# Optimization experiments

Hardware: AMD Instinct MI355X
Metric: run time of the kernel (lower is better)

## Reference

```python
import jax, jax.numpy as jnp
import numpy as np

N = 50000    # total nodes in a batched graph
E = 200000   # directed edges (before self loops)
G = 256      # molecules per batch
F_IN = 64    # atom features
H = 4        # gat heads
CH = 128     # hidden_channels (per head)
D = H * CH   # 512, concat width
MLP_H = 128  # hidden_channels * mlp_hidden_factor
NEG_SLOPE = 0.2


def _gat(x, src, dst, W, a_src, a_dst, b, concat):
    """PyG GATConv (eval mode, self loops already added to src/dst)."""
    n = x.shape[0]
    heads, ch = a_src.shape
    h = (x @ W).reshape(n, heads, ch)                       # [N,H,C]
    e = jax.nn.leaky_relu((h * a_src).sum(-1)[src]
                          + (h * a_dst).sum(-1)[dst], NEG_SLOPE)  # [E,H]
    emax = jax.ops.segment_max(e, dst, num_segments=n)
    emax = jnp.where(jnp.isfinite(emax), emax, 0.0)
    p = jnp.exp(e - emax[dst])
    denom = jax.ops.segment_sum(p, dst, num_segments=n)
    alpha = p / (denom[dst] + 1e-16)                        # segment softmax over dst
    out = jax.ops.segment_sum(h[src] * alpha[..., None], dst, num_segments=n)
    out = out.reshape(n, heads * ch) if concat else out.mean(axis=1)
    return out + b


def _encoder(x, edge_index, batch, p):
    n = x.shape[0]
    loop = jnp.arange(n, dtype=edge_index.dtype)            # GATConv add_self_loops=True
    src = jnp.concatenate([edge_index[0], loop])
    dst = jnp.concatenate([edge_index[1], loop])
    x = jax.nn.elu(_gat(x, src, dst, p['W1'], p['as1'], p['ad1'], p['b1'], True))
    x = jax.nn.elu(_gat(x, src, dst, p['W2'], p['as2'], p['ad2'], p['b2'], True))
    x = _gat(x, src, dst, p['W3'], p['as3'], p['ad3'], p['b3'], False)
    emb = jax.ops.segment_max(x, batch, num_segments=G)     # global_max_pool
    return jnp.where(jnp.isfinite(emb), emb, 0.0)


def setup_inputs() -> dict:
    key = jax.random.key(0)
    ks = jax.random.split(key, 24)
    rn = lambda k, s, sc=0.1: jax.random.normal(k, s, jnp.float32) * sc
    return dict(
        x1=rn(ks[0], (N, F_IN), 1.0),
        edge_index1=jax.random.randint(ks[1], (2, E), 0, N, dtype=jnp.int32),
        batch1=jnp.sort(jax.random.randint(ks[2], (N,), 0, G, dtype=jnp.int32)),
        x2=rn(ks[3], (N, F_IN), 1.0),
        edge_index2=jax.random.randint(ks[4], (2, E), 0, N, dtype=jnp.int32),
        batch2=jnp.sort(jax.random.randint(ks[5], (N,), 0, G, dtype=jnp.int32)),
        W1=rn(ks[6], (F_IN, D)), as1=rn(ks[7], (H, CH)), ad1=rn(ks[8], (H, CH)),
        b1=jnp.zeros((D,), jnp.float32),
        W2=rn(ks[9], (D, D)), as2=rn(ks[10], (H, CH)), ad2=rn(ks[11], (H, CH)),
        b2=jnp.zeros((D,), jnp.float32),
        W3=rn(ks[12], (D, CH)), as3=rn(ks[13], (1, CH)), ad3=rn(ks[14], (1, CH)),
        b3=jnp.zeros((CH,), jnp.float32),
        mw1=rn(ks[15], (2 * CH, MLP_H)), mb1=jnp.zeros((MLP_H,), jnp.float32),
        mw2=rn(ks[16], (MLP_H, 1)), mb2=jnp.zeros((1,), jnp.float32),
    )


def reference(x1, edge_index1, batch1, x2, edge_index2, batch2,
              W1, as1, ad1, b1, W2, as2, ad2, b2, W3, as3, ad3, b3,
              mw1, mb1, mw2, mb2):
    p = dict(W1=W1, as1=as1, ad1=ad1, b1=b1,
             W2=W2, as2=as2, ad2=ad2, b2=b2,
             W3=W3, as3=as3, ad3=ad3, b3=b3)
    e1 = _encoder(x1, edge_index1, batch1, p)               # [G, CH]
    e2 = _encoder(x2, edge_index2, batch2, p)               # [G, CH]
    z = jnp.concatenate([e1, e2], axis=-1)                  # [G, 2*CH]
    return jax.nn.relu(z @ mw1 + mb1) @ mw2 + mb2           # [G, 1]
```

## Files before the change

### kernel.cpp

```cpp
#include <hip/hip_runtime.h>
#include <cstdint>

namespace {
constexpr int kN = 50000;
constexpr int kE = 200000;
constexpr int kE2 = kE + kN;
constexpr int kG = 256;
constexpr float kNegSlope = 0.2f;
}

using half8   = __attribute__((ext_vector_type(8))) _Float16;
using floatx4 = __attribute__((ext_vector_type(4))) float;

__device__ __forceinline__ void gld_lds16(const void* g, void* l) {
  __builtin_amdgcn_global_load_lds(
      (const __attribute__((address_space(1))) unsigned int*)g,
      (__attribute__((address_space(3))) unsigned int*)l, 16, 0, 0);
}

__device__ __forceinline__ float fexp(float x) {
  return __builtin_amdgcn_exp2f(x * 1.44269504088896f);
}

template <int OUTF16, int BN, int CT>
__global__ __launch_bounds__(512, 2) void gemm256(
    const _Float16* __restrict__ A, const _Float16* __restrict__ B,
    void* __restrict__ Cv, int M, int N, int K) {
  constexpr int ASLOTS = 2048;
  constexpr int BSLOTS = BN * 8;
  constexpr int LPT = (ASLOTS + BSLOTS) / 512;
  constexpr int BUFB = (ASLOTS + BSLOTS) * 16;
  constexpr int WN = (BN == 256) ? 4 : 2;
  constexpr int WM = 8 / WN;
  constexpr int WTM = 256 / WM;
  constexpr int WTN = BN / WN;
  constexpr int MI = WTM / 16;
  constexpr int NI = WTN / 16;
  __shared__ alignas(16) char smem[2 * BUFB];
  const int t = threadIdx.x;
  const int w = t >> 6, l = t & 63;
  const int x = blockIdx.x & 7, s = blockIdx.x >> 3;
  const int col = (CT == 1) ? 0 : (s & (CT - 1));
  const int rt = ((CT == 1) ? s : (s >> 1)) * 8 + x;
  const int bm = rt * 256;
  const int bn = col * BN;
  if (bm >= M) return;
  const int wr = w / WN, wc = w % WN;
  const int quad = l >> 4, lrow = l & 15;

  floatx4 acc[MI][NI];
#pragma unroll
  for (int mi = 0; mi < MI; ++mi)
#pragma unroll
    for (int ni = 0; ni < NI; ++ni) acc[mi][ni] = (floatx4){0.f, 0.f, 0.f, 0.f};

  auto stage = [&](char* buf, int k0) {
#pragma unroll
    for (int i = 0; i < ASLOTS / 512; ++i) {
      const int sl = i * 512 + t;
      const int kh = sl >> 10;
      const int r = sl & 1023;
      const int row = ((r >> 6) << 4) + (r & 15);
      const int q = (r >> 4) & 3;
      int ga = bm + row;
      ga = (ga < M) ? ga : (M - 1);
      gld_lds16(A + (size_t)ga * K + k0 + kh * 32 + q * 8, buf + sl * 16);
    }
#pragma unroll
    for (int i = 0; i < BSLOTS / 512; ++i) {
      const int sl = i * 512 + t;
      const int kh = sl / (BSLOTS / 2);
      const int r = sl % (BSLOTS / 2);
      const int row = ((r >> 6) << 4) + (r & 15);
      const int q = (r >> 4) & 3;
      gld_lds16(B + (size_t)(bn + row) * K + k0 + kh * 32 + q * 8,
                buf + (ASLOTS + sl) * 16);
    }
  };

  stage(smem, 0);
  int cur = 0;
  for (int k0 = 0; k0 < K; k0 += 64) {
    char* bufc = smem + cur * BUFB;
    if (k0 + 64 < K) {
      stage(smem + (cur ^ 1) * BUFB, k0 + 64);
      if constexpr (LPT == 8)
        asm volatile("s_waitcnt vmcnt(8)" ::: "memory");
      else
        asm volatile("s_waitcnt vmcnt(6)" ::: "memory");
    } else {
      asm volatile("s_waitcnt vmcnt(0)" ::: "memory");
    }
    __builtin_amdgcn_s_barrier();
    asm volatile("" ::: "memory");
#pragma unroll
    for (int kh = 0; kh < 2; ++kh) {
      half8 fa[MI], fb[NI];
#pragma unroll
      for (int mi = 0; mi < MI; ++mi)
        fa[mi] = *(const half8*)(bufc + ((kh * 16 + wr * MI + mi) << 10) + l * 16);
#pragma unroll
      for (int ni = 0; ni < NI; ++ni)
        fb[ni] = *(const half8*)(bufc + ASLOTS * 16 +
                                 ((kh * (BN / 16) + wc * NI + ni) << 10) + l * 16);
      __builtin_amdgcn_s_setprio(1);
#pragma unroll
      for (int mi = 0; mi < MI; ++mi)
#pragma unroll
        for (int ni = 0; ni < NI; ++ni)
          acc[mi][ni] = __builtin_amdgcn_mfma_f32_16x16x32_f16(
              fa[mi], fb[ni], acc[mi][ni], 0, 0, 0);
      __builtin_amdgcn_s_setprio(0);
    }
    asm volatile("" ::: "memory");
    __builtin_amdgcn_s_barrier();
    cur ^= 1;
  }
  const int colbase = bn + wc * WTN + lrow;
#pragma unroll
  for (int mi = 0; mi < MI; ++mi) {
    const int rbase = bm + wr * WTM + mi * 16 + quad * 4;
#pragma unroll
    for (int r = 0; r < 4; ++r) {
      const int grow = rbase + r;
      if (grow < M) {
        if constexpr (OUTF16) {
          _Float16* C = (_Float16*)Cv;
#pragma unroll
          for (int ni = 0; ni < NI; ++ni)
            C[(size_t)grow * N + colbase + ni * 16] = (_Float16)acc[mi][ni][r];
        } else {
          float* C = (float*)Cv;
#pragma unroll
          for (int ni = 0; ni < NI; ++ni)
            C[(size_t)grow * N + colbase + ni * 16] = acc[mi][ni][r];
        }
      }
    }
  }
}

__global__ void wt_split_all(const float* __restrict__ W1, _Float16* Th1,
                             const float* __restrict__ W2, _Float16* Th2,
                             const float* __restrict__ W3, _Float16* Th3) {
  int idx = blockIdx.x * blockDim.x + threadIdx.x;
  const float* W;
  _Float16* Th;
  int K, N;
  if (idx < 64 * 512) {
    W = W1; Th = Th1; K = 64; N = 512;
  } else if (idx < 64 * 512 + 512 * 512) {
    idx -= 64 * 512;
    W = W2; Th = Th2; K = 512; N = 512;
  } else if (idx < 64 * 512 + 512 * 512 + 512 * 128) {
    idx -= 64 * 512 + 512 * 512;
    W = W3; Th = Th3; K = 512; N = 128;
  } else {
    return;
  }
  const int k = idx / N;
  const int n = idx - k * N;
  Th[n * K + k] = (_Float16)W[idx];
}

__global__ void prep2(const float* __restrict__ x0, const float* __restrict__ x1,
                      _Float16* __restrict__ Xh, int* __restrict__ cnt,
                      int* __restrict__ total) {
  const int idx = blockIdx.x * blockDim.x + threadIdx.x;
  const int half = kN * 64;
  if (idx < half) Xh[idx] = (_Float16)x0[idx];
  else if (idx < 2 * half) Xh[idx] = (_Float16)x1[idx - half];
  if (idx < 2 * kN) cnt[idx] = 1;
  if (idx == 0) *total = 0;
}
__global__ void prep(const float* __restrict__ X, _Float16* __restrict__ Xh,
                     int* __restrict__ cnt, int* __restrict__ total, int nsplit,
                     int n) {
  const int idx = blockIdx.x * blockDim.x + threadIdx.x;
  if (idx < nsplit) Xh[idx] = (_Float16)X[idx];
  if (idx < n) cnt[idx] = 1;
  if (idx == 0) *total = 0;
}

__global__ void count_edges2(const int* __restrict__ d0, const int* __restrict__ d1,
                             int* __restrict__ cnt) {
  const int i = blockIdx.x * blockDim.x + threadIdx.x;
  if (i < kE) atomicAdd(&cnt[d0[i]], 1);
  else if (i < 2 * kE) atomicAdd(&cnt[d1[i - kE] + kN], 1);
}
__global__ void fill_edges2(const int* __restrict__ s0, const int* __restrict__ d0,
                            const int* __restrict__ s1, const int* __restrict__ d1,
                            int* __restrict__ cursor, int* __restrict__ csr) {
  const int i = blockIdx.x * blockDim.x + threadIdx.x;
  if (i < kE) {
    const int p = atomicAdd(&cursor[d0[i]], 1);
    csr[p] = s0[i];
  } else if (i < 2 * kE) {
    const int j = i - kE;
    const int p = atomicAdd(&cursor[d1[j] + kN], 1);
    csr[p] = s1[j] + kN;
  }
}
__global__ void count_edges(const int* __restrict__ dst, int* __restrict__ cnt,
                            int ne) {
  const int i = blockIdx.x * blockDim.x + threadIdx.x;
  if (i < ne) atomicAdd(&cnt[dst[i]], 1);
}
__global__ void fill_edges(const int* __restrict__ src, const int* __restrict__ dst,
                           int* __restrict__ cursor, int* __restrict__ csr, int ne) {
  const int i = blockIdx.x * blockDim.x + threadIdx.x;
  if (i < ne) {
    const int p = atomicAdd(&cursor[dst[i]], 1);
    csr[p] = src[i];
  }
}
__global__ void alloc_ranges(const int* __restrict__ cnt, int* __restrict__ start,
                             int* __restrict__ cursor, int* __restrict__ total,
                             int* __restrict__ csr, int n) {
  const int i = blockIdx.x * blockDim.x + threadIdx.x;
  const int lane = threadIdx.x & 63;
  const int v = (i < n) ? cnt[i] : 0;
  int sc = v;
#pragma unroll
  for (int off = 1; off < 64; off <<= 1) {
    const int t = __shfl_up(sc, off);
    if (lane >= off) sc += t;
  }
  const int wtot = __shfl(sc, 63);
  int base = 0;
  if (lane == 63) base = atomicAdd(total, wtot);
  base = __shfl(base, 63);
  const int st = base + sc - v;
  if (i < n) {
    start[i] = st;
    cursor[i] = st + 1;
    csr[st] = i;
  }
}

__global__ void gat_agg4(const _Float16* __restrict__ h,
                         const float* __restrict__ a_src,
                         const float* __restrict__ a_dst,
                         const int* __restrict__ start, const int* __restrict__ cnt,
                         const int* __restrict__ csr_src,
                         const float* __restrict__ bias,
                         _Float16* __restrict__ outH, int n_nodes) {
  const int gtid = blockIdx.x * blockDim.x + threadIdx.x;
  const int node = gtid >> 6;
  const int lane = threadIdx.x & 63;
  if (node >= n_nodes) return;
  const int ch = lane * 8;
  float as_r[8], ad_r[8];
#pragma unroll
  for (int j = 0; j < 8; ++j) {
    as_r[j] = a_src[ch + j];
    ad_r[j] = a_dst[ch + j];
  }
  const int s = start[node];
  const int c = cnt[node];
  const half8 vs = *(const half8*)(h + (size_t)node * 512 + ch);
  float fs[8];
  float t_src = 0.f, t_dst = 0.f;
#pragma unroll
  for (int j = 0; j < 8; ++j) {
    fs[j] = (float)vs[j];
    t_src = fmaf(fs[j], as_r[j], t_src);
    t_dst = fmaf(fs[j], ad_r[j], t_dst);
  }
#pragma unroll
  for (int off = 1; off < 16; off <<= 1) {
    t_src += __shfl_xor(t_src, off);
    t_dst += __shfl_xor(t_dst, off);
  }
  const float ad = t_dst;
  float es = t_src + ad;
  es = (es > 0.f) ? es : kNegSlope * es;
  const float ws = fexp(es);
  float d0 = ws, d1 = 0.f;
  float a0[8], a1[8];
#pragma unroll
  for (int j = 0; j < 8; ++j) {
    a0[j] = ws * fs[j];
    a1[j] = 0.f;
  }
  int i = 1;
  for (; i + 2 <= c; i += 2) {
    const int s0 = csr_src[s + i];
    const int s1 = csr_src[s + i + 1];
    const half8 v0 = *(const half8*)(h + (size_t)s0 * 512 + ch);
    const half8 v1 = *(const half8*)(h + (size_t)s1 * 512 + ch);
    float f0[8], f1[8];
    float t0 = 0.f, t1 = 0.f;
#pragma unroll
    for (int j = 0; j < 8; ++j) {
      f0[j] = (float)v0[j];
      f1[j] = (float)v1[j];
      t0 = fmaf(f0[j], as_r[j], t0);
      t1 = fmaf(f1[j], as_r[j], t1);
    }
#pragma unroll
    for (int off = 1; off < 16; off <<= 1) {
      t0 += __shfl_xor(t0, off);
      t1 += __shfl_xor(t1, off);
    }
    float e0 = t0 + ad;
    float e1 = t1 + ad;
    e0 = (e0 > 0.f) ? e0 : kNegSlope * e0;
    e1 = (e1 > 0.f) ? e1 : kNegSlope * e1;
    const float w0 = fexp(e0);
    const float w1 = fexp(e1);
    d0 += w0;
    d1 += w1;
#pragma unroll
    for (int j = 0; j < 8; ++j) {
      a0[j] = fmaf(w0, f0[j], a0[j]);
      a1[j] = fmaf(w1, f1[j], a1[j]);
    }
  }
  if (i < c) {
    const int s0 = csr_src[s + i];
    const half8 v0 = *(const half8*)(h + (size_t)s0 * 512 + ch);
    float f0[8];
    float t0 = 0.f;
#pragma unroll
    for (int j = 0; j < 8; ++j) {
      f0[j] = (float)v0[j];
      t0 = fmaf(f0[j], as_r[j], t0);
    }
#pragma unroll
    for (int off = 1; off < 16; off <<= 1) t0 += __shfl_xor(t0, off);
    float e0 = t0 + ad;
    e0 = (e0 > 0.f) ? e0 : kNegSlope * e0;
    const float w0 = fexp(e0);
    d0 += w0;
#pragma unroll
    for (int j = 0; j < 8; ++j) a0[j] = fmaf(w0, f0[j], a0[j]);
  }
  const float inv = 1.f / (d0 + d1 + 1e-16f);
  half8 H;
#pragma unroll
  for (int j = 0; j < 8; ++j) {
    float v = (a0[j] + a1[j]) * inv + bias[ch + j];
    v = (v > 0.f) ? v : (fexp(v) - 1.f);
    H[j] = (_Float16)v;
  }
  *(half8*)(outH + (size_t)node * 512 + ch) = H;
}

__global__ void gat_agg_l3(const float* __restrict__ h,
                           const float* __restrict__ a_src,
                           const float* __restrict__ a_dst,
                           const int* __restrict__ start, const int* __restrict__ cnt,
                           const int* __restrict__ csr_src,
                           const float* __restrict__ bias,
                           float* __restrict__ out, int n_nodes) {
  const int gtid = blockIdx.x * blockDim.x + threadIdx.x;
  const int node = gtid >> 6;
  const int lane = threadIdx.x & 63;
  if (node >= n_nodes) return;
  const float2 asv = *(const float2*)(a_src + lane * 2);
  const float2 adv = *(const float2*)(a_dst + lane * 2);
  const int s = start[node];
  const int c = cnt[node];
  const float2 vs = *(const float2*)(h + (size_t)node * 128 + lane * 2);
  float t_src = fmaf(vs.x, asv.x, vs.y * asv.y);
  float t_dst = fmaf(vs.x, adv.x, vs.y * adv.y);
#pragma unroll
  for (int off = 1; off < 64; off <<= 1) {
    t_src += __shfl_xor(t_src, off);
    t_dst += __shfl_xor(t_dst, off);
  }
  const float ad = t_dst;
  float es = t_src + ad;
  es = (es > 0.f) ? es : kNegSlope * es;
  const float ws = fexp(es);
  float2 a0 = make_float2(ws * vs.x, ws * vs.y);
  float2 a1 = make_float2(0.f, 0.f);
  float d0 = ws, d1 = 0.f;
  int i = 1;
  for (; i + 2 <= c; i += 2) {
    const int s0 = csr_src[s + i];
    const int s1 = csr_src[s + i + 1];
    const float2 v0 = *(const float2*)(h + (size_t)s0 * 128 + lane * 2);
    const float2 v1 = *(const float2*)(h + (size_t)s1 * 128 + lane * 2);
    float t0 = fmaf(v0.x, asv.x, v0.y * asv.y);
    float t1 = fmaf(v1.x, asv.x, v1.y * asv.y);
#pragma unroll
    for (int off = 1; off < 64; off <<= 1) {
      t0 += __shfl_xor(t0, off);
      t1 += __shfl_xor(t1, off);
    }
    float e0 = t0 + ad;
    float e1 = t1 + ad;
    e0 = (e0 > 0.f) ? e0 : kNegSlope * e0;
    e1 = (e1 > 0.f) ? e1 : kNegSlope * e1;
    const float w0 = fexp(e0);
    const float w1 = fexp(e1);
    d0 += w0;
    d1 += w1;
    a0.x = fmaf(w0, v0.x, a0.x); a1.x = fmaf(w1, v1.x, a1.x);
    a0.y = fmaf(w0, v0.y, a0.y); a1.y = fmaf(w1, v1.y, a1.y);
  }
  if (i < c) {
    const int s0 = csr_src[s + i];
    const float2 v0 = *(const float2*)(h + (size_t)s0 * 128 + lane * 2);
    float t0 = fmaf(v0.x, asv.x, v0.y * asv.y);
#pragma unroll
    for (int off = 1; off < 64; off <<= 1) t0 += __shfl_xor(t0, off);
    float e0 = t0 + ad;
    e0 = (e0 > 0.f) ? e0 : kNegSlope * e0;
    const float w0 = fexp(e0);
    d0 += w0;
    a0.x = fmaf(w0, v0.x, a0.x);
    a0.y = fmaf(w0, v0.y, a0.y);
  }
  const float inv = 1.f / (d0 + d1 + 1e-16f);
  *(float2*)(out + (size_t)node * 128 + lane * 2) =
      make_float2((a0.x + a1.x) * inv + bias[lane * 2],
                  (a0.y + a1.y) * inv + bias[lane * 2 + 1]);
}

__global__ void pool_max(const float* __restrict__ x, const int* __restrict__ batch,
                         float* __restrict__ emb, int n_nodes) {
  __shared__ int lohi[2];
  const int g = blockIdx.x;
  if (threadIdx.x == 0) {
    int lo = 0, hi = n_nodes;
    while (lo < hi) {
      const int mid = (lo + hi) >> 1;
      if (batch[mid] < g) lo = mid + 1; else hi = mid;
    }
    lohi[0] = lo;
    hi = n_nodes;
    while (lo < hi) {
      const int mid = (lo + hi) >> 1;
      if (batch[mid] < g + 1) lo = mid + 1; else hi = mid;
    }
    lohi[1] = lo;
  }
  __syncthreads();
  const int lo = lohi[0], hi = lohi[1];
  const int c = threadIdx.x;
  float m = -1e30f;
  for (int nid = lo; nid < hi; ++nid) m = fmaxf(m, x[(size_t)nid * 128 + c]);
  emb[g * 128 + c] = (lo < hi) ? m : 0.f;
}

__global__ void mlp_head(const float* __restrict__ e1, const float* __restrict__ e2,
                         const float* __restrict__ mw1, const float* __restrict__ mb1,
                         const float* __restrict__ mw2, const float* __restrict__ mb2,
                         float* __restrict__ out) {
  __shared__ float z[256];
  __shared__ float red[128];
  const int g = blockIdx.x;
  const int j = threadIdx.x;
  z[j] = e1[g * 128 + j];
  z[j + 128] = e2[g * 128 + j];
  __syncthreads();
  float acc = mb1[j];
  for (int k = 0; k < 256; ++k) acc = fmaf(z[k], mw1[k * 128 + j], acc);
  acc = fmaxf(acc, 0.f) * mw2[j];
  red[j] = acc;
  __syncthreads();
  for (int s = 64; s > 0; s >>= 1) {
    if (j < s) red[j] += red[j + s];
    __syncthreads();
  }
  if (j == 0) out[g] = red[0] + mb2[0];
}

namespace {
struct Bufs {
  _Float16 *R1h, *R2h;
  float *R1f, *R2f, *asrc, *adst;
  int *cnt, *start, *cursor, *csr, *total;
  _Float16 *Wth1, *Wth2, *Wth3;
  float* emb;
  size_t need;
};

Bufs plan(void* d_ws, int M, int E) {
  Bufs b;
  char* w = (char*)d_ws;
  size_t off = 0;
  auto take = [&](size_t bytes) -> void* {
    void* p = w + off;
    off += (bytes + 255) & ~(size_t)255;
    return p;
  };
  b.R1h = (_Float16*)take((size_t)M * 512 * 2);
  b.R1f = (float*)b.R1h;
  b.R2h = (_Float16*)take((size_t)M * 512 * 2);
  b.R2f = (float*)b.R2h;
  b.asrc = (float*)take((size_t)M * 4 * 4);
  b.adst = (float*)take((size_t)M * 4 * 4);
  b.cnt = (int*)take((size_t)M * 4);
  b.start = (int*)take((size_t)M * 4);
  b.cursor = (int*)take((size_t)M * 4);
  b.csr = (int*)take((size_t)E * 4);
  b.total = (int*)take(256);
  b.Wth1 = (_Float16*)take((size_t)64 * 512 * 2);
  b.Wth2 = (_Float16*)take((size_t)512 * 512 * 2);
  b.Wth3 = (_Float16*)take((size_t)512 * 128 * 2);
  b.emb = (float*)take((size_t)2 * kG * 128 * 4);
  b.need = off;
  return b;
}

void run_layers(const Bufs& b, void* const* d_in, int M, hipStream_t stream) {
  const float* as1 = (const float*)d_in[7];
  const float* ad1 = (const float*)d_in[8];
  const float* b1 = (const float*)d_in[9];
  const float* as2 = (const float*)d_in[11];
  const float* ad2 = (const float*)d_in[12];
  const float* b2 = (const float*)d_in[13];
  const float* as3 = (const float*)d_in[15];
  const float* ad3 = (const float*)d_in[16];
  const float* b3 = (const float*)d_in[17];
  const int nodeBlocks = (M * 64) / 256;
  const int MT = (M + 255) / 256;
  const int SP = (MT + 7) / 8;

  gemm256<1, 256, 2><<<SP * 16, 512, 0, stream>>>(b.R1h, b.Wth1, b.R2h, M, 512, 64);
  gat_agg4<<<nodeBlocks, 256, 0, stream>>>(b.R2h, as1, ad1, b.start, b.cnt,
                                           b.csr, b1, b.R1h, M);
  gemm256<1, 256, 2><<<SP * 16, 512, 0, stream>>>(b.R1h, b.Wth2, b.R2h, M, 512, 512);
  gat_agg4<<<nodeBlocks, 256, 0, stream>>>(b.R2h, as2, ad2, b.start, b.cnt,
                                           b.csr, b2, b.R1h, M);
  gemm256<0, 128, 1><<<SP * 8, 512, 0, stream>>>(b.R1h, b.Wth3, b.R2f, M, 128, 512);
  gat_agg_l3<<<nodeBlocks, 256, 0, stream>>>(b.R2f, as3, ad3, b.start, b.cnt,
                                             b.csr, b3, b.R1f, M);
}
}

extern "C" void kernel_launch(void* const* d_in, const int* in_sizes, int n_in,
                              void* d_out, int out_size, void* d_ws, size_t ws_size,
                              hipStream_t stream) {
  (void)in_sizes; (void)n_in; (void)out_size;
  const float* W1 = (const float*)d_in[6];
  const float* W2 = (const float*)d_in[10];
  const float* W3 = (const float*)d_in[14];
  const float* mw1 = (const float*)d_in[18];
  const float* mb1 = (const float*)d_in[19];
  const float* mw2 = (const float*)d_in[20];
  const float* mb2 = (const float*)d_in[21];

  Bufs bc = plan(d_ws, 2 * kN, 2 * kE2);
  const bool combined = bc.need <= ws_size;
  Bufs b = combined ? bc : plan(d_ws, kN, kE2);

  const int wtot = 64 * 512 + 512 * 512 + 512 * 128;
  wt_split_all<<<(wtot + 255) / 256, 256, 0, stream>>>(W1, b.Wth1, W2, b.Wth2, W3,
                                                       b.Wth3);
  if (combined) {
    const int M = 2 * kN;
    const int* ei0 = (const int*)d_in[1];
    const int* ei1 = (const int*)d_in[4];
    prep2<<<(2 * kN * 64 + 255) / 256, 256, 0, stream>>>(
        (const float*)d_in[0], (const float*)d_in[3], b.R1h, b.cnt, b.total);
    count_edges2<<<(2 * kE + 255) / 256, 256, 0, stream>>>(ei0 + kE, ei1 + kE,
                                                           b.cnt);
    alloc_ranges<<<(M + 255) / 256, 256, 0, stream>>>(b.cnt, b.start, b.cursor,
                                                      b.total, b.csr, M);
    fill_edges2<<<(2 * kE + 255) / 256, 256, 0, stream>>>(ei0, ei0 + kE, ei1,
                                                          ei1 + kE, b.cursor, b.csr);
    run_layers(b, d_in, M, stream);
    for (int enc = 0; enc < 2; ++enc) {
      const int* batch = (const int*)d_in[enc * 3 + 2];
      pool_max<<<kG, 128, 0, stream>>>(b.R1f + (size_t)enc * kN * 128, batch,
                                       b.emb + (size_t)enc * kG * 128, kN);
    }
  } else {
    for (int enc = 0; enc < 2; ++enc) {
      const float* x = (const float*)d_in[enc * 3 + 0];
      const int* ei = (const int*)d_in[enc * 3 + 1];
      const int* batch = (const int*)d_in[enc * 3 + 2];
      prep<<<(kN * 64 + 255) / 256, 256, 0, stream>>>(x, b.R1h, b.cnt, b.total,
                                                      kN * 64, kN);
      count_edges<<<(kE + 255) / 256, 256, 0, stream>>>(ei + kE, b.cnt, kE);
      alloc_ranges<<<(kN + 255) / 256, 256, 0, stream>>>(b.cnt, b.start, b.cursor,
                                                         b.total, b.csr, kN);
      fill_edges<<<(kE + 255) / 256, 256, 0, stream>>>(ei, ei + kE, b.cursor, b.csr,
                                                       kE);
      run_layers(b, d_in, kN, stream);
      pool_max<<<kG, 128, 0, stream>>>(b.R1f, batch, b.emb + (size_t)enc * kG * 128,
                                       kN);
    }
  }
  mlp_head<<<kG, 128, 0, stream>>>(b.emb, b.emb + (size_t)kG * 128, mw1, mb1, mw2,
                                   mb2, (float*)d_out);
}
```

Before: 695.5 us.

## Replace double-buffered GEMM with 4-slot ring pipeline and merge pool launches

The GEMM now stages K in 32-wide tiles through a 4-deep LDS ring, prefetching three tiles ahead. It splits the A and B loads around two halves of the MFMA work so memory traffic overlaps compute more finely. The two per-encoder pool_max launches are also merged into a single pool_max2 launch. The deeper ring keeps the same LDS size but doubles the barriers per unit of K and depends on hand-tuned vmcnt counts, so a miscount would silently corrupt results.

New measurement: 671.9 us. 1.04x faster.

```diff
diff --git a/kernel.cpp b/kernel.cpp
--- a/kernel.cpp
+++ b/kernel.cpp
@@ -23,20 +23,20 @@
 }
 
 template <int OUTF16, int BN, int CT>
-__global__ __launch_bounds__(512, 2) void gemm256(
+__global__ __launch_bounds__(512, 2) void gemm_ring(
     const _Float16* __restrict__ A, const _Float16* __restrict__ B,
     void* __restrict__ Cv, int M, int N, int K) {
-  constexpr int ASLOTS = 2048;
-  constexpr int BSLOTS = BN * 8;
-  constexpr int LPT = (ASLOTS + BSLOTS) / 512;
-  constexpr int BUFB = (ASLOTS + BSLOTS) * 16;
+  constexpr int ASL = 1024;
+  constexpr int BSL = BN * 4;
+  constexpr int SLOT = (ASL + BSL) * 16;
+  constexpr int LPT = (ASL + BSL) / 512;
   constexpr int WN = (BN == 256) ? 4 : 2;
   constexpr int WM = 8 / WN;
   constexpr int WTM = 256 / WM;
   constexpr int WTN = BN / WN;
   constexpr int MI = WTM / 16;
   constexpr int NI = WTN / 16;
-  __shared__ alignas(16) char smem[2 * BUFB];
+  __shared__ alignas(16) char smem[4 * SLOT];
   const int t = threadIdx.x;
   const int w = t >> 6, l = t & 63;
   const int x = blockIdx.x & 7, s = blockIdx.x >> 3;
@@ -54,68 +54,78 @@
 #pragma unroll
     for (int ni = 0; ni < NI; ++ni) acc[mi][ni] = (floatx4){0.f, 0.f, 0.f, 0.f};
 
-  auto stage = [&](char* buf, int k0) {
-#pragma unroll
-    for (int i = 0; i < ASLOTS / 512; ++i) {
+  auto stageA = [&](int kt) {
+    char* buf = smem + (size_t)(kt & 3) * SLOT;
+    int k0 = kt * 32;
+    k0 = (k0 > K - 32) ? (K - 32) : k0;
+#pragma unroll
+    for (int i = 0; i < 2; ++i) {
       const int sl = i * 512 + t;
-      const int kh = sl >> 10;
-      const int r = sl & 1023;
-      const int row = ((r >> 6) << 4) + (r & 15);
-      const int q = (r >> 4) & 3;
+      const int row = ((sl >> 6) << 4) + (sl & 15);
+      const int q = (sl >> 4) & 3;
       int ga = bm + row;
       ga = (ga < M) ? ga : (M - 1);
-      gld_lds16(A + (size_t)ga * K + k0 + kh * 32 + q * 8, buf + sl * 16);
-    }
-#pragma unroll
-    for (int i = 0; i < BSLOTS / 512; ++i) {
+      gld_lds16(A + (size_t)ga * K + k0 + q * 8, buf + sl * 16);
+    }
+  };
+  auto stageB = [&](int kt) {
+    char* buf = smem + (size_t)(kt & 3) * SLOT + ASL * 16;
+    int k0 = kt * 32;
+    k0 = (k0 > K - 32) ? (K - 32) : k0;
+#pragma unroll
+    for (int i = 0; i < LPT - 2; ++i) {
       const int sl = i * 512 + t;
-      const int kh = sl / (BSLOTS / 2);
-      const int r = sl % (BSLOTS / 2);
-      const int row = ((r >> 6) << 4) + (r & 15);
-      const int q = (r >> 4) & 3;
-      gld_lds16(B + (size_t)(bn + row) * K + k0 + kh * 32 + q * 8,
-                buf + (ASLOTS + sl) * 16);
+      const int row = ((sl >> 6) << 4) + (sl & 15);
+      const int q = (sl >> 4) & 3;
+      gld_lds16(B + (size_t)(bn + row) * K + k0 + q * 8, buf + sl * 16);
     }
   };
 
-  stage(smem, 0);
-  int cur = 0;
-  for (int k0 = 0; k0 < K; k0 += 64) {
-    char* bufc = smem + cur * BUFB;
-    if (k0 + 64 < K) {
-      stage(smem + (cur ^ 1) * BUFB, k0 + 64);
-      if constexpr (LPT == 8)
-        asm volatile("s_waitcnt vmcnt(8)" ::: "memory");
-      else
-        asm volatile("s_waitcnt vmcnt(6)" ::: "memory");
-    } else {
-      asm volatile("s_waitcnt vmcnt(0)" ::: "memory");
-    }
+  stageA(0); stageB(0);
+  stageA(1); stageB(1);
+  stageA(2); stageB(2);
+
+  const int NT = K >> 5;
+  for (int kt = 0; kt < NT; ++kt) {
+    char* bufc = smem + (size_t)(kt & 3) * SLOT;
+    stageA(kt + 3);
+    if constexpr (BN == 256)
+      asm volatile("s_waitcnt vmcnt(10)" ::: "memory");
+    else
+      asm volatile("s_waitcnt vmcnt(8)" ::: "memory");
     __builtin_amdgcn_s_barrier();
     asm volatile("" ::: "memory");
-#pragma unroll
-    for (int kh = 0; kh < 2; ++kh) {
-      half8 fa[MI], fb[NI];
-#pragma unroll
-      for (int mi = 0; mi < MI; ++mi)
-        fa[mi] = *(const half8*)(bufc + ((kh * 16 + wr * MI + mi) << 10) + l * 16);
+    half8 fa[MI], fb[NI];
+#pragma unroll
+    for (int ni = 0; ni < NI; ++ni)
+      fb[ni] = *(const half8*)(bufc + ASL * 16 + ((wc * NI + ni) << 10) + l * 16);
+#pragma unroll
+    for (int mi = 0; mi < MI / 2; ++mi)
+      fa[mi] = *(const half8*)(bufc + ((wr * MI + mi) << 10) + l * 16);
+    __builtin_amdgcn_s_setprio(1);
+#pragma unroll
+    for (int mi = 0; mi < MI / 2; ++mi)
 #pragma unroll
       for (int ni = 0; ni < NI; ++ni)
-        fb[ni] = *(const half8*)(bufc + ASLOTS * 16 +
-                                 ((kh * (BN / 16) + wc * NI + ni) << 10) + l * 16);
-      __builtin_amdgcn_s_setprio(1);
-#pragma unroll
-      for (int mi = 0; mi < MI; ++mi)
-#pragma unroll
-        for (int ni = 0; ni < NI; ++ni)
-          acc[mi][ni] = __builtin_amdgcn_mfma_f32_16x16x32_f16(
-              fa[mi], fb[ni], acc[mi][ni], 0, 0, 0);
-      __builtin_amdgcn_s_setprio(0);
-    }
+        acc[mi][ni] = __builtin_amdgcn_mfma_f32_16x16x32_f16(
+            fa[mi], fb[ni], acc[mi][ni], 0, 0, 0);
+    __builtin_amdgcn_s_setprio(0);
+    stageB(kt + 3);
+#pragma unroll
+    for (int mi = MI / 2; mi < MI; ++mi)
+      fa[mi] = *(const half8*)(bufc + ((wr * MI + mi) << 10) + l * 16);
+    __builtin_amdgcn_s_setprio(1);
+#pragma unroll
+    for (int mi = MI / 2; mi < MI; ++mi)
+#pragma unroll
+      for (int ni = 0; ni < NI; ++ni)
+        acc[mi][ni] = __builtin_amdgcn_mfma_f32_16x16x32_f16(
+            fa[mi], fb[ni], acc[mi][ni], 0, 0, 0);
+    __builtin_amdgcn_s_setprio(0);
     asm volatile("" ::: "memory");
     __builtin_amdgcn_s_barrier();
-    cur ^= 1;
-  }
+  }
+  asm volatile("s_waitcnt vmcnt(0)" ::: "memory");
   const int colbase = bn + wc * WTN + lrow;
 #pragma unroll
   for (int mi = 0; mi < MI; ++mi) {
@@ -420,6 +430,34 @@
                   (a0.y + a1.y) * inv + bias[lane * 2 + 1]);
 }
 
+__global__ void pool_max2(const float* __restrict__ x, const int* __restrict__ bt1,
+                          const int* __restrict__ bt2, float* __restrict__ emb) {
+  __shared__ int lohi[2];
+  const int enc = blockIdx.x >> 8;
+  const int g = blockIdx.x & 255;
+  const int* batch = enc ? bt2 : bt1;
+  const float* xx = x + (size_t)enc * kN * 128;
+  if (threadIdx.x == 0) {
+    int lo = 0, hi = kN;
+    while (lo < hi) {
+      const int mid = (lo + hi) >> 1;
+      if (batch[mid] < g) lo = mid + 1; else hi = mid;
+    }
+    lohi[0] = lo;
+    hi = kN;
+    while (lo < hi) {
+      const int mid = (lo + hi) >> 1;
+      if (batch[mid] < g + 1) lo = mid + 1; else hi = mid;
+    }
+    lohi[1] = lo;
+  }
+  __syncthreads();
+  const int lo = lohi[0], hi = lohi[1];
+  const int c = threadIdx.x;
+  float m = -1e30f;
+  for (int nid = lo; nid < hi; ++nid) m = fmaxf(m, xx[(size_t)nid * 128 + c]);
+  emb[(size_t)blockIdx.x * 128 + c] = (lo < hi) ? m : 0.f;
+}
 __global__ void pool_max(const float* __restrict__ x, const int* __restrict__ batch,
                          float* __restrict__ emb, int n_nodes) {
   __shared__ int lohi[2];
@@ -521,13 +559,13 @@
   const int MT = (M + 255) / 256;
   const int SP = (MT + 7) / 8;
 
-  gemm256<1, 256, 2><<<SP * 16, 512, 0, stream>>>(b.R1h, b.Wth1, b.R2h, M, 512, 64);
+  gemm_ring<1, 256, 2><<<SP * 16, 512, 0, stream>>>(b.R1h, b.Wth1, b.R2h, M, 512, 64);
   gat_agg4<<<nodeBlocks, 256, 0, stream>>>(b.R2h, as1, ad1, b.start, b.cnt,
                                            b.csr, b1, b.R1h, M);
-  gemm256<1, 256, 2><<<SP * 16, 512, 0, stream>>>(b.R1h, b.Wth2, b.R2h, M, 512, 512);
+  gemm_ring<1, 256, 2><<<SP * 16, 512, 0, stream>>>(b.R1h, b.Wth2, b.R2h, M, 512, 512);
   gat_agg4<<<nodeBlocks, 256, 0, stream>>>(b.R2h, as2, ad2, b.start, b.cnt,
                                            b.csr, b2, b.R1h, M);
-  gemm256<0, 128, 1><<<SP * 8, 512, 0, stream>>>(b.R1h, b.Wth3, b.R2f, M, 128, 512);
+  gemm_ring<0, 128, 1><<<SP * 8, 512, 0, stream>>>(b.R1h, b.Wth3, b.R2f, M, 128, 512);
   gat_agg_l3<<<nodeBlocks, 256, 0, stream>>>(b.R2f, as3, ad3, b.start, b.cnt,
                                              b.csr, b3, b.R1f, M);
 }
@@ -565,11 +603,8 @@
     fill_edges2<<<(2 * kE + 255) / 256, 256, 0, stream>>>(ei0, ei0 + kE, ei1,
                                                           ei1 + kE, b.cursor, b.csr);
     run_layers(b, d_in, M, stream);
-    for (int enc = 0; enc < 2; ++enc) {
-      const int* batch = (const int*)d_in[enc * 3 + 2];
-      pool_max<<<kG, 128, 0, stream>>>(b.R1f + (size_t)enc * kN * 128, batch,
-                                       b.emb + (size_t)enc * kG * 128, kN);
-    }
+    pool_max2<<<2 * kG, 128, 0, stream>>>(b.R1f, (const int*)d_in[2],
+                                          (const int*)d_in[5], b.emb);
   } else {
     for (int enc = 0; enc < 2; ++enc) {
       const float* x = (const float*)d_in[enc * 3 + 0];
```
